# Kernel tuning notes

Measured on AMD Instinct MI355X. Metric: run time of the kernel, lower is better.

Reference implementation:

```python
import jax, jax.numpy as jnp
import numpy as np

I_DIM = 50000
D_DIM = 128
N_EDGES = 800000
N_NODES = I_DIM + 1


def setup_inputs() -> dict:
    key = jax.random.key(0)
    k1, k2, k3, k4 = jax.random.split(key, 4)
    # edge[:,0] must be sorted for the original bincount+repeat normalization to be valid
    src = jnp.sort(jax.random.randint(k1, (N_EDGES,), 0, N_NODES))
    dst = jax.random.randint(k2, (N_EDGES,), 0, N_NODES)
    edge = jnp.stack([src, dst], axis=1).astype(jnp.int64)
    # GlorotNormal-style init for the embedding table and dense layers
    emb_mat = jax.random.normal(k3, (N_NODES, D_DIM), dtype=jnp.float32) * np.sqrt(2.0 / (N_NODES + D_DIM))
    kA, kB = jax.random.split(k4)
    W_scale = jax.random.normal(kA, (D_DIM, D_DIM), dtype=jnp.float32) * np.sqrt(2.0 / (2 * D_DIM))
    b_scale = jnp.zeros((D_DIM,), dtype=jnp.float32)
    W_att = jax.random.normal(kB, (2 * D_DIM, 1), dtype=jnp.float32) * np.sqrt(2.0 / (2 * D_DIM + 1))
    b_att = jnp.zeros((1,), dtype=jnp.float32)
    return {"edge": edge, "emb_mat": emb_mat, "W_scale": W_scale,
            "b_scale": b_scale, "W_att": W_att, "b_att": b_att}


def reference(edge, emb_mat, W_scale, b_scale, W_att, b_att):
    E = edge.shape[0]
    src = edge[:, 0]
    dst = edge[:, 1]
    # gather both endpoints, project: [E, 2, d]
    edge_emb = jnp.einsum('epd,df->epf', emb_mat[edge], W_scale) + b_scale
    edge_emb = edge_emb.reshape(E, -1)                       # [E, 2d]
    att = edge_emb @ W_att + b_att                           # [E, 1]
    att = jnp.where(att >= 0, att, 0.2 * att)                # LeakyReLU(0.2)
    att = jnp.squeeze(att, axis=-1)                          # [E]
    scores = jnp.exp(att - 1.0)
    score_sum = jax.ops.segment_sum(scores, src, num_segments=N_NODES)
    score_norm = scores / score_sum[src]                     # segment softmax
    item_scaled = emb_mat @ W_scale + b_scale                # [N, d]
    msgs = score_norm[:, None] * item_scaled[dst]            # [E, d]
    agg = jax.ops.segment_sum(msgs, src, num_segments=N_NODES)
    return jax.nn.sigmoid(agg)                               # [N, d]
```

## Files before the change

kernel.cpp:

```cpp
#include <hip/hip_runtime.h>
#include <math.h>

#define NN 50001
#define DD 128
#define NE 800000
#define GEMM_BLOCKS 782
#define EDGE_BLOCKS 3125
#define WSTRIDE 132

typedef __attribute__((ext_vector_type(8))) short short8;
typedef __attribute__((ext_vector_type(4))) float floatx4;

__device__ __forceinline__ unsigned short f2bf(float f) {
    unsigned u = __builtin_bit_cast(unsigned, f);
    u += 0x7fffu + ((u >> 16) & 1u);
    return (unsigned short)(u >> 16);
}
__device__ __forceinline__ float bflo(unsigned u) {
    return __builtin_bit_cast(float, u << 16);
}
__device__ __forceinline__ float bfhi(unsigned u) {
    return __builtin_bit_cast(float, u & 0xffff0000u);
}
__device__ __forceinline__ float score(float att) {
    att = att >= 0.f ? att : 0.2f * att;
    return __expf(att - 1.f);
}

__global__ void __launch_bounds__(256) k_gemm(const float* __restrict__ emb,
        const float* __restrict__ W, const float* __restrict__ b_scale,
        const float* __restrict__ W_att, const int* __restrict__ edge,
        unsigned short* __restrict__ item, float* __restrict__ a_src,
        float* __restrict__ a_dst, int* __restrict__ row_ptr,
        const float* __restrict__ b_att) {
    if (blockIdx.x >= GEMM_BLOCKS) {
        int e = (blockIdx.x - GEMM_BLOCKS) * 256 + threadIdx.x;
        if (e >= NE) return;
        int s = edge[2 * e];
        if (e == 0) {
            for (int n = 0; n <= s; n++) row_ptr[n] = 0;
        } else {
            int p = edge[2 * (e - 1)];
            for (int n = p + 1; n <= s; n++) row_ptr[n] = e;
        }
        if (e == NE - 1) {
            for (int n = s + 1; n <= NN; n++) row_ptr[n] = NE;
        }
        return;
    }
    __shared__ unsigned short WTl[DD * WSTRIDE];
    {
        const float4* Wv = (const float4*)W;
        #pragma unroll
        for (int it = 0; it < 16; it++) {
            int f = it * 256 + threadIdx.x;
            int k = f >> 5;
            int j4 = (f & 31) * 4;
            float4 w = Wv[f];
            WTl[(j4 + 0) * WSTRIDE + k] = f2bf(w.x);
            WTl[(j4 + 1) * WSTRIDE + k] = f2bf(w.y);
            WTl[(j4 + 2) * WSTRIDE + k] = f2bf(w.z);
            WTl[(j4 + 3) * WSTRIDE + k] = f2bf(w.w);
        }
    }
    __syncthreads();

    int wave = blockIdx.x * 4 + (threadIdx.x >> 6);
    int lane = threadIdx.x & 63;
    int base = wave * 16;
    if (base >= NN) return;
    int m = lane & 15, q = lane >> 4;
    int node = base + m;
    bool valid = node < NN;

    int row = valid ? node : NN - 1;
    const float* bp = emb + (long)row * DD + q * 8;
    short8 b[4];
    #pragma unroll
    for (int ks = 0; ks < 4; ks++) {
        float4 f0 = *(const float4*)(bp + ks * 32);
        float4 f1 = *(const float4*)(bp + ks * 32 + 4);
        b[ks][0] = (short)f2bf(f0.x); b[ks][1] = (short)f2bf(f0.y);
        b[ks][2] = (short)f2bf(f0.z); b[ks][3] = (short)f2bf(f0.w);
        b[ks][4] = (short)f2bf(f1.x); b[ks][5] = (short)f2bf(f1.y);
        b[ks][6] = (short)f2bf(f1.z); b[ks][7] = (short)f2bf(f1.w);
    }

    float p_src = 0.f, p_dst = 0.f;

    #pragma unroll
    for (int ft = 0; ft < 8; ft++) {
        floatx4 acc = {0.f, 0.f, 0.f, 0.f};
        const unsigned short* wrow = WTl + (ft * 16 + m) * WSTRIDE;
        #pragma unroll
        for (int ks = 0; ks < 4; ks++) {
            short8 a = *(const short8*)(wrow + ks * 32 + q * 8);
            acc = __builtin_amdgcn_mfma_f32_16x16x32_bf16(a, b[ks], acc, 0, 0, 0);
        }
        int fo = ft * 16 + q * 4;
        float4 bs = *(const float4*)(b_scale + fo);
        float4 ws = *(const float4*)(W_att + fo);
        float4 wd = *(const float4*)(W_att + DD + fo);
        float v0 = acc[0] + bs.x, v1 = acc[1] + bs.y;
        float v2 = acc[2] + bs.z, v3 = acc[3] + bs.w;
        if (valid) {
            uint2 pk;
            pk.x = (unsigned)f2bf(v0) | ((unsigned)f2bf(v1) << 16);
            pk.y = (unsigned)f2bf(v2) | ((unsigned)f2bf(v3) << 16);
            *(uint2*)(item + (long)node * DD + fo) = pk;
        }
        p_src += v0 * ws.x + v1 * ws.y + v2 * ws.z + v3 * ws.w;
        p_dst += v0 * wd.x + v1 * wd.y + v2 * wd.z + v3 * wd.w;
    }
    p_src += __shfl_xor(p_src, 16, 64); p_src += __shfl_xor(p_src, 32, 64);
    p_dst += __shfl_xor(p_dst, 16, 64); p_dst += __shfl_xor(p_dst, 32, 64);
    if (q == 0 && valid) { a_src[node] = p_src + b_att[0]; a_dst[node] = p_dst; }
}

__global__ void __launch_bounds__(256) k_agg(const int* __restrict__ edge,
        const int* __restrict__ row_ptr, const unsigned short* __restrict__ item,
        const float* __restrict__ a_src, const float* __restrict__ a_dst,
        float* __restrict__ out) {
    int n = blockIdx.x * 4 + (threadIdx.x >> 6);
    int lane = threadIdx.x & 63;
    if (n >= NN) return;
    int g = lane >> 4, t = lane & 15;

    int start = row_ptr[n];
    int len = row_ptr[n + 1] - start;
    const int* dp = edge + 2 * start + 1;

    if (len > 0) {
        float asrc = a_src[n];
        float acc[8] = {0.f, 0.f, 0.f, 0.f, 0.f, 0.f, 0.f, 0.f};
        float ssum = 0.f;
        int j = g;
        for (; j + 12 < len; j += 16) {
            int d0 = dp[2 * j], d1 = dp[2 * (j + 4)], d2 = dp[2 * (j + 8)], d3 = dp[2 * (j + 12)];
            float x0 = a_dst[d0], x1 = a_dst[d1], x2 = a_dst[d2], x3 = a_dst[d3];
            uint4 u0 = *(const uint4*)(item + (long)d0 * DD + t * 8);
            uint4 u1 = *(const uint4*)(item + (long)d1 * DD + t * 8);
            uint4 u2 = *(const uint4*)(item + (long)d2 * DD + t * 8);
            uint4 u3 = *(const uint4*)(item + (long)d3 * DD + t * 8);
            float s0 = score(asrc + x0), s1 = score(asrc + x1);
            float s2 = score(asrc + x2), s3 = score(asrc + x3);
            ssum += (s0 + s1) + (s2 + s3);
            acc[0] += s0 * bflo(u0.x); acc[1] += s0 * bfhi(u0.x);
            acc[2] += s0 * bflo(u0.y); acc[3] += s0 * bfhi(u0.y);
            acc[4] += s0 * bflo(u0.z); acc[5] += s0 * bfhi(u0.z);
            acc[6] += s0 * bflo(u0.w); acc[7] += s0 * bfhi(u0.w);
            acc[0] += s1 * bflo(u1.x); acc[1] += s1 * bfhi(u1.x);
            acc[2] += s1 * bflo(u1.y); acc[3] += s1 * bfhi(u1.y);
            acc[4] += s1 * bflo(u1.z); acc[5] += s1 * bfhi(u1.z);
            acc[6] += s1 * bflo(u1.w); acc[7] += s1 * bfhi(u1.w);
            acc[0] += s2 * bflo(u2.x); acc[1] += s2 * bfhi(u2.x);
            acc[2] += s2 * bflo(u2.y); acc[3] += s2 * bfhi(u2.y);
            acc[4] += s2 * bflo(u2.z); acc[5] += s2 * bfhi(u2.z);
            acc[6] += s2 * bflo(u2.w); acc[7] += s2 * bfhi(u2.w);
            acc[0] += s3 * bflo(u3.x); acc[1] += s3 * bfhi(u3.x);
            acc[2] += s3 * bflo(u3.y); acc[3] += s3 * bfhi(u3.y);
            acc[4] += s3 * bflo(u3.z); acc[5] += s3 * bfhi(u3.z);
            acc[6] += s3 * bflo(u3.w); acc[7] += s3 * bfhi(u3.w);
        }
        for (; j < len; j += 4) {
            int d = dp[2 * j];
            float x = a_dst[d];
            uint4 u = *(const uint4*)(item + (long)d * DD + t * 8);
            float s = score(asrc + x);
            ssum += s;
            acc[0] += s * bflo(u.x); acc[1] += s * bfhi(u.x);
            acc[2] += s * bflo(u.y); acc[3] += s * bfhi(u.y);
            acc[4] += s * bflo(u.z); acc[5] += s * bfhi(u.z);
            acc[6] += s * bflo(u.w); acc[7] += s * bfhi(u.w);
        }
        #pragma unroll
        for (int off = 16; off <= 32; off <<= 1) {
            #pragma unroll
            for (int k = 0; k < 8; k++) acc[k] += __shfl_xor(acc[k], off, 64);
            ssum += __shfl_xor(ssum, off, 64);
        }
        float inv = 1.f / ssum;
        float4 o;
        if (g == 0) {
            o.x = 1.f / (1.f + __expf(-acc[0] * inv));
            o.y = 1.f / (1.f + __expf(-acc[1] * inv));
            o.z = 1.f / (1.f + __expf(-acc[2] * inv));
            o.w = 1.f / (1.f + __expf(-acc[3] * inv));
            *(float4*)(out + (long)n * DD + t * 8) = o;
        } else if (g == 1) {
            o.x = 1.f / (1.f + __expf(-acc[4] * inv));
            o.y = 1.f / (1.f + __expf(-acc[5] * inv));
            o.z = 1.f / (1.f + __expf(-acc[6] * inv));
            o.w = 1.f / (1.f + __expf(-acc[7] * inv));
            *(float4*)(out + (long)n * DD + t * 8 + 4) = o;
        }
    } else {
        float4 h = make_float4(0.5f, 0.5f, 0.5f, 0.5f);
        if (g == 0)      *(float4*)(out + (long)n * DD + t * 8) = h;
        else if (g == 1) *(float4*)(out + (long)n * DD + t * 8 + 4) = h;
    }
}

extern "C" void kernel_launch(void* const* d_in, const int* in_sizes, int n_in,
                              void* d_out, int out_size, void* d_ws, size_t ws_size,
                              hipStream_t stream) {
    const int*   edge    = (const int*)d_in[0];
    const float* emb     = (const float*)d_in[1];
    const float* W_scale = (const float*)d_in[2];
    const float* b_scale = (const float*)d_in[3];
    const float* W_att   = (const float*)d_in[4];
    const float* b_att   = (const float*)d_in[5];
    float* out = (float*)d_out;

    char* ws = (char*)d_ws;
    int*            row_ptr = (int*)(ws);
    float*          a_src   = (float*)(ws + 200832);
    float*          a_dst   = (float*)(ws + 401024);
    unsigned short* item    = (unsigned short*)(ws + 601216);

    int node_blocks = (NN + 3) / 4;

    k_gemm <<<GEMM_BLOCKS + EDGE_BLOCKS, 256, 0, stream>>>(emb, W_scale, b_scale, W_att,
                                                           edge, item, a_src, a_dst,
                                                           row_ptr, b_att);
    k_agg  <<<node_blocks,               256, 0, stream>>>(edge, row_ptr, item,
                                                           a_src, a_dst, out);
}
```

Before: 141.1 us.

## Assign one 16-lane group per node and share edge scores via shuffles

The aggregation kernel now maps each node to a 16-thread group instead of a full 64-lane wavefront, so a block covers 16 nodes rather than 4. Within a group, each lane loads one edge's destination index and computes its score, and these are broadcast with width-16 shuffles before every lane gathers its 8-feature slice of each neighbour row. This removes the cross-group reduction of the accumulators and the idle lanes in the final store. With an average degree of about 16 it should make better use of lanes, at the cost of serial per-edge gathers inside a group and extra shuffle instructions.

Result: faster. 137.4 us (-2.6%).

```diff
diff --git a/kernel.cpp b/kernel.cpp
--- a/kernel.cpp
+++ b/kernel.cpp
@@ -117,88 +117,88 @@
     if (q == 0 && valid) { a_src[node] = p_src + b_att[0]; a_dst[node] = p_dst; }
 }
 
+#define ACC8(S, U) \
+    acc[0] += (S) * bflo((U).x); acc[1] += (S) * bfhi((U).x); \
+    acc[2] += (S) * bflo((U).y); acc[3] += (S) * bfhi((U).y); \
+    acc[4] += (S) * bflo((U).z); acc[5] += (S) * bfhi((U).z); \
+    acc[6] += (S) * bflo((U).w); acc[7] += (S) * bfhi((U).w);
+
 __global__ void __launch_bounds__(256) k_agg(const int* __restrict__ edge,
         const int* __restrict__ row_ptr, const unsigned short* __restrict__ item,
         const float* __restrict__ a_src, const float* __restrict__ a_dst,
         float* __restrict__ out) {
-    int n = blockIdx.x * 4 + (threadIdx.x >> 6);
-    int lane = threadIdx.x & 63;
+    int n = blockIdx.x * 16 + (threadIdx.x >> 4);
+    int t = threadIdx.x & 15;
     if (n >= NN) return;
-    int g = lane >> 4, t = lane & 15;
 
     int start = row_ptr[n];
     int len = row_ptr[n + 1] - start;
+    float* op = out + (long)n * DD + t * 8;
+
+    if (len <= 0) {
+        float4 h = make_float4(0.5f, 0.5f, 0.5f, 0.5f);
+        *(float4*)op = h;
+        *(float4*)(op + 4) = h;
+        return;
+    }
+
+    float asrc = a_src[n];
     const int* dp = edge + 2 * start + 1;
-
-    if (len > 0) {
-        float asrc = a_src[n];
-        float acc[8] = {0.f, 0.f, 0.f, 0.f, 0.f, 0.f, 0.f, 0.f};
-        float ssum = 0.f;
-        int j = g;
-        for (; j + 12 < len; j += 16) {
-            int d0 = dp[2 * j], d1 = dp[2 * (j + 4)], d2 = dp[2 * (j + 8)], d3 = dp[2 * (j + 12)];
-            float x0 = a_dst[d0], x1 = a_dst[d1], x2 = a_dst[d2], x3 = a_dst[d3];
-            uint4 u0 = *(const uint4*)(item + (long)d0 * DD + t * 8);
-            uint4 u1 = *(const uint4*)(item + (long)d1 * DD + t * 8);
-            uint4 u2 = *(const uint4*)(item + (long)d2 * DD + t * 8);
-            uint4 u3 = *(const uint4*)(item + (long)d3 * DD + t * 8);
-            float s0 = score(asrc + x0), s1 = score(asrc + x1);
-            float s2 = score(asrc + x2), s3 = score(asrc + x3);
-            ssum += (s0 + s1) + (s2 + s3);
-            acc[0] += s0 * bflo(u0.x); acc[1] += s0 * bfhi(u0.x);
-            acc[2] += s0 * bflo(u0.y); acc[3] += s0 * bfhi(u0.y);
-            acc[4] += s0 * bflo(u0.z); acc[5] += s0 * bfhi(u0.z);
-            acc[6] += s0 * bflo(u0.w); acc[7] += s0 * bfhi(u0.w);
-            acc[0] += s1 * bflo(u1.x); acc[1] += s1 * bfhi(u1.x);
-            acc[2] += s1 * bflo(u1.y); acc[3] += s1 * bfhi(u1.y);
-            acc[4] += s1 * bflo(u1.z); acc[5] += s1 * bfhi(u1.z);
-            acc[6] += s1 * bflo(u1.w); acc[7] += s1 * bfhi(u1.w);
-            acc[0] += s2 * bflo(u2.x); acc[1] += s2 * bfhi(u2.x);
-            acc[2] += s2 * bflo(u2.y); acc[3] += s2 * bfhi(u2.y);
-            acc[4] += s2 * bflo(u2.z); acc[5] += s2 * bfhi(u2.z);
-            acc[6] += s2 * bflo(u2.w); acc[7] += s2 * bfhi(u2.w);
-            acc[0] += s3 * bflo(u3.x); acc[1] += s3 * bfhi(u3.x);
-            acc[2] += s3 * bflo(u3.y); acc[3] += s3 * bfhi(u3.y);
-            acc[4] += s3 * bflo(u3.z); acc[5] += s3 * bfhi(u3.z);
-            acc[6] += s3 * bflo(u3.w); acc[7] += s3 * bfhi(u3.w);
-        }
-        for (; j < len; j += 4) {
-            int d = dp[2 * j];
-            float x = a_dst[d];
-            uint4 u = *(const uint4*)(item + (long)d * DD + t * 8);
-            float s = score(asrc + x);
-            ssum += s;
-            acc[0] += s * bflo(u.x); acc[1] += s * bfhi(u.x);
-            acc[2] += s * bflo(u.y); acc[3] += s * bfhi(u.y);
-            acc[4] += s * bflo(u.z); acc[5] += s * bfhi(u.z);
-            acc[6] += s * bflo(u.w); acc[7] += s * bfhi(u.w);
-        }
-        #pragma unroll
-        for (int off = 16; off <= 32; off <<= 1) {
-            #pragma unroll
-            for (int k = 0; k < 8; k++) acc[k] += __shfl_xor(acc[k], off, 64);
-            ssum += __shfl_xor(ssum, off, 64);
-        }
-        float inv = 1.f / ssum;
-        float4 o;
-        if (g == 0) {
-            o.x = 1.f / (1.f + __expf(-acc[0] * inv));
-            o.y = 1.f / (1.f + __expf(-acc[1] * inv));
-            o.z = 1.f / (1.f + __expf(-acc[2] * inv));
-            o.w = 1.f / (1.f + __expf(-acc[3] * inv));
-            *(float4*)(out + (long)n * DD + t * 8) = o;
-        } else if (g == 1) {
-            o.x = 1.f / (1.f + __expf(-acc[4] * inv));
-            o.y = 1.f / (1.f + __expf(-acc[5] * inv));
-            o.z = 1.f / (1.f + __expf(-acc[6] * inv));
-            o.w = 1.f / (1.f + __expf(-acc[7] * inv));
-            *(float4*)(out + (long)n * DD + t * 8 + 4) = o;
-        }
-    } else {
-        float4 h = make_float4(0.5f, 0.5f, 0.5f, 0.5f);
-        if (g == 0)      *(float4*)(out + (long)n * DD + t * 8) = h;
-        else if (g == 1) *(float4*)(out + (long)n * DD + t * 8 + 4) = h;
-    }
+    const unsigned short* ip = item + t * 8;
+
+    float acc[8] = {0.f, 0.f, 0.f, 0.f, 0.f, 0.f, 0.f, 0.f};
+    float ssum = 0.f;
+
+    for (int j = 0; j < len; j += 16) {
+        int jj = j + t;
+        int idx = jj < len ? jj : len - 1;
+        int d = dp[2 * idx];
+        float x = a_dst[d];
+        float s = (jj < len) ? score(asrc + x) : 0.f;
+        ssum += s;
+
+        int cnt = len - j;
+        if (cnt > 16) cnt = 16;
+        int kk = 0;
+        for (; kk + 4 <= cnt; kk += 4) {
+            int d0 = __shfl(d, kk, 16),     d1 = __shfl(d, kk + 1, 16);
+            int d2 = __shfl(d, kk + 2, 16), d3 = __shfl(d, kk + 3, 16);
+            float s0 = __shfl(s, kk, 16),     s1 = __shfl(s, kk + 1, 16);
+            float s2 = __shfl(s, kk + 2, 16), s3 = __shfl(s, kk + 3, 16);
+            uint4 u0 = *(const uint4*)(ip + (long)d0 * DD);
+            uint4 u1 = *(const uint4*)(ip + (long)d1 * DD);
+            uint4 u2 = *(const uint4*)(ip + (long)d2 * DD);
+            uint4 u3 = *(const uint4*)(ip + (long)d3 * DD);
+            ACC8(s0, u0);
+            ACC8(s1, u1);
+            ACC8(s2, u2);
+            ACC8(s3, u3);
+        }
+        for (; kk < cnt; kk++) {
+            int d0 = __shfl(d, kk, 16);
+            float s0 = __shfl(s, kk, 16);
+            uint4 u0 = *(const uint4*)(ip + (long)d0 * DD);
+            ACC8(s0, u0);
+        }
+    }
+
+    ssum += __shfl_xor(ssum, 1, 16);
+    ssum += __shfl_xor(ssum, 2, 16);
+    ssum += __shfl_xor(ssum, 4, 16);
+    ssum += __shfl_xor(ssum, 8, 16);
+    float inv = 1.f / ssum;
+
+    float4 o0, o1;
+    o0.x = 1.f / (1.f + __expf(-acc[0] * inv));
+    o0.y = 1.f / (1.f + __expf(-acc[1] * inv));
+    o0.z = 1.f / (1.f + __expf(-acc[2] * inv));
+    o0.w = 1.f / (1.f + __expf(-acc[3] * inv));
+    o1.x = 1.f / (1.f + __expf(-acc[4] * inv));
+    o1.y = 1.f / (1.f + __expf(-acc[5] * inv));
+    o1.z = 1.f / (1.f + __expf(-acc[6] * inv));
+    o1.w = 1.f / (1.f + __expf(-acc[7] * inv));
+    *(float4*)op = o0;
+    *(float4*)(op + 4) = o1;
 }
 
 extern "C" void kernel_launch(void* const* d_in, const int* in_sizes, int n_in,
@@ -218,7 +218,7 @@
     float*          a_dst   = (float*)(ws + 401024);
     unsigned short* item    = (unsigned short*)(ws + 601216);
 
-    int node_blocks = (NN + 3) / 4;
+    int node_blocks = (NN + 15) / 16;
 
     k_gemm <<<GEMM_BLOCKS + EDGE_BLOCKS, 256, 0, stream>>>(emb, W_scale, b_scale, W_att,
                                                            edge, item, a_src, a_dst,
```
